# Optimization experiments

Hardware: AMD Instinct MI355X
Metric: run time of the kernel (lower is better)

## Reference

```python
import jax, jax.numpy as jnp
import numpy as np

B, D, T = 8, 1024, 512
HID, NH, NL = 256, 4, 2
OUT = HID // NH  # 64 per-head dim
ALPHA = 0.2      # leaky relu slope
EPS = 1e-5       # layernorm eps


def setup_inputs() -> dict:
    key = jax.random.key(0)
    ks = jax.random.split(key, 10)
    X_obs = jax.random.normal(ks[0], (B, D, T), dtype=jnp.float32)
    mask = (jax.random.uniform(ks[1], (B, D, T)) < 0.8).astype(jnp.float32)
    W_in = jax.random.normal(ks[2], (2 * T, HID), dtype=jnp.float32) * (1.0 / np.sqrt(2 * T))
    b_in = jnp.zeros((HID,), dtype=jnp.float32)
    gat_W = jax.random.normal(ks[3], (NL, NH, HID, OUT), dtype=jnp.float32) * (1.0 / np.sqrt(HID))
    gat_a = jax.random.normal(ks[4], (NL, NH, 2 * OUT), dtype=jnp.float32) * 0.1
    ln_g = jnp.ones((NL, HID), dtype=jnp.float32)
    ln_b = jnp.zeros((NL, HID), dtype=jnp.float32)
    W_out = jax.random.normal(ks[5], (HID, T), dtype=jnp.float32) * (1.0 / np.sqrt(HID))
    b_out = jnp.zeros((T,), dtype=jnp.float32)
    return dict(X_obs=X_obs, mask=mask, W_in=W_in, b_in=b_in, gat_W=gat_W,
                gat_a=gat_a, ln_g=ln_g, ln_b=ln_b, W_out=W_out, b_out=b_out)


def _layer_norm(x, g, b):
    mu = jnp.mean(x, axis=-1, keepdims=True)
    var = jnp.mean((x - mu) ** 2, axis=-1, keepdims=True)
    return (x - mu) * jax.lax.rsqrt(var + EPS) * g + b


def _gat_forward(X_obs, mask, W_in, b_in, gat_W, gat_a, ln_g, ln_b, W_out, b_out):
    # mean-impute per (d, t) position across batch
    obs_sum = jnp.sum(X_obs * mask, axis=0, keepdims=True)
    obs_cnt = jnp.sum(mask, axis=0, keepdims=True)
    pos_mean = obs_sum / (obs_cnt + 1e-10)
    X_mean = X_obs * mask + (1.0 - mask) * pos_mean

    x = jnp.concatenate([X_mean, mask], axis=-1)       # (B, D, 2T)
    h = x @ W_in + b_in                                 # (B, N, HID)

    for l in range(NL):
        Wl = gat_W[l]                                   # (H, HID, OUT)
        a_left = gat_a[l, :, :OUT]                      # (H, OUT)
        a_right = gat_a[l, :, OUT:]                     # (H, OUT)
        hW = jnp.einsum('bnd,hde->bhne', h, Wl)         # (B, H, N, OUT)
        # e_ij = leakyrelu(a_left . h_i + a_right . h_j) -- avoids O(N^2 * 2d) concat
        s_l = jnp.einsum('bhne,he->bhn', hW, a_left)
        s_r = jnp.einsum('bhne,he->bhn', hW, a_right)
        e = jax.nn.leaky_relu(s_l[..., :, None] + s_r[..., None, :], ALPHA)  # (B,H,N,N)
        attn = jax.nn.softmax(e, axis=-1)
        head_out = jnp.einsum('bhnm,bhme->bhne', attn, hW)                   # (B,H,N,OUT)
        h_new = jnp.transpose(head_out, (0, 2, 1, 3)).reshape(h.shape[0], h.shape[1], HID)
        h = _layer_norm(h + h_new, ln_g[l], ln_b[l])

    return h @ W_out + b_out                            # (B, D, T)


def reference(X_obs, mask, W_in, b_in, gat_W, gat_a, ln_g, ln_b, W_out, b_out):
    return _gat_forward(X_obs, mask, W_in, b_in, gat_W, gat_a, ln_g, ln_b, W_out, b_out)
```

## Files before the change

### kernel.cpp

```cpp
#include <hip/hip_runtime.h>
#include <hip/hip_bf16.h>

constexpr int B_   = 8;
constexpr int D_   = 1024;
constexpr int T_   = 512;
constexpr int HID_ = 256;
constexpr int NH_  = 4;
constexpr int NL_  = 2;
constexpr float ALPHA_ = 0.2f;
constexpr float EPS_   = 1e-5f;
constexpr int OUT_ = 64;
constexpr int M_ = B_ * D_;
constexpr int DT_ = D_ * T_;
constexpr int KIN_ = 2 * T_;

typedef __attribute__((ext_vector_type(8))) short short8;
typedef __attribute__((ext_vector_type(4))) float floatx4;

__device__ __forceinline__ unsigned short f2bf(float f) {
    unsigned int u = __float_as_uint(f);
    unsigned int r = u + 0x7fffu + ((u >> 16) & 1u);
    return (unsigned short)(r >> 16);
}
__device__ __forceinline__ float bf2f(unsigned short u) {
    return __uint_as_float((unsigned int)u << 16);
}
__device__ __forceinline__ unsigned int kenc(float f) {
    unsigned int u = __float_as_uint(f);
    return (u & 0x80000000u) ? ~u : (u | 0x80000000u);
}
__device__ __forceinline__ float kdec(unsigned int k) {
    unsigned int u = (k & 0x80000000u) ? (k ^ 0x80000000u) : ~k;
    return __uint_as_float(u);
}
__device__ __forceinline__ void gll16(const unsigned short* g, unsigned short* l) {
    __builtin_amdgcn_global_load_lds(
        (const __attribute__((address_space(1))) void*)g,
        (__attribute__((address_space(3))) void*)l, 16, 0, 0);
}

__global__ __launch_bounds__(256) void impute_k(const float* __restrict__ X,
                                                const float* __restrict__ Mk,
                                                unsigned short* __restrict__ Ain) {
    int idx4 = (blockIdx.x * 256 + threadIdx.x) * 4;
    int t = idx4 & (T_ - 1);
    int d = idx4 >> 9;
    float4 x[B_], m[B_];
    float4 s = {0, 0, 0, 0}, c = {0, 0, 0, 0};
#pragma unroll
    for (int b = 0; b < B_; b++) {
        x[b] = *(const float4*)&X[(size_t)b * DT_ + idx4];
        m[b] = *(const float4*)&Mk[(size_t)b * DT_ + idx4];
        s.x += x[b].x * m[b].x; s.y += x[b].y * m[b].y;
        s.z += x[b].z * m[b].z; s.w += x[b].w * m[b].w;
        c.x += m[b].x; c.y += m[b].y; c.z += m[b].z; c.w += m[b].w;
    }
    float4 pm;
    pm.x = s.x / (c.x + 1e-10f); pm.y = s.y / (c.y + 1e-10f);
    pm.z = s.z / (c.z + 1e-10f); pm.w = s.w / (c.w + 1e-10f);
#pragma unroll
    for (int b = 0; b < B_; b++) {
        size_t row = (size_t)b * D_ + d;
        ushort4 xm, mk;
        xm.x = f2bf(x[b].x * m[b].x + (1.f - m[b].x) * pm.x);
        xm.y = f2bf(x[b].y * m[b].y + (1.f - m[b].y) * pm.y);
        xm.z = f2bf(x[b].z * m[b].z + (1.f - m[b].z) * pm.z);
        xm.w = f2bf(x[b].w * m[b].w + (1.f - m[b].w) * pm.w);
        mk.x = f2bf(m[b].x); mk.y = f2bf(m[b].y);
        mk.z = f2bf(m[b].z); mk.w = f2bf(m[b].w);
        *(ushort4*)&Ain[row * KIN_ + t]      = xm;
        *(ushort4*)&Ain[row * KIN_ + T_ + t] = mk;
    }
}

__global__ __launch_bounds__(256) void wprep_k(const float* __restrict__ W_in,
                                               const float* __restrict__ gatW,
                                               const float* __restrict__ W_out,
                                               unsigned short* __restrict__ Wt_in,
                                               unsigned short* __restrict__ Wcat,
                                               unsigned short* __restrict__ WtO,
                                               unsigned int* __restrict__ rmaxkey) {
    int idx = blockIdx.x * 256 + threadIdx.x;
    if (idx < 64) rmaxkey[idx] = 0u;
    if (idx < 262144) {
        int n = idx >> 10, k = idx & 1023;
        Wt_in[idx] = f2bf(W_in[(size_t)k * HID_ + n]);
    } else if (idx < 393216) {
        int j = idx - 262144;
        int l = j >> 16, n = (j >> 8) & 255, k = j & 255;
        int h = n >> 6, e = n & 63;
        Wcat[j] = f2bf(gatW[(((size_t)(l * NH_ + h) * HID_) + k) * OUT_ + e]);
    } else {
        int j = idx - 393216;
        int n = j >> 8, k = j & 255;
        WtO[j] = f2bf(W_out[(size_t)k * T_ + n]);
    }
}

template <int MODE>
__global__ __launch_bounds__(256) void gemm_bf16_k(
        const unsigned short* __restrict__ A,
        const unsigned short* __restrict__ Bt,
        const float* __restrict__ bias,
        float* __restrict__ C,
        unsigned short* __restrict__ Cb,
        const float* __restrict__ ga,
        float* __restrict__ s_l,
        float* __restrict__ s_r,
        unsigned int* __restrict__ rmaxkey,
        int Nsz, int Ksz) {
    __shared__ __align__(16) unsigned short As[2][128 * 32];
    __shared__ __align__(16) unsigned short Bs[2][64 * 32];
    int tid = threadIdx.x;
    int wave = tid >> 6, lane = tid & 63;
    int q = lane >> 4, r16 = lane & 15;
    int rowbase = blockIdx.y * 128;
    int colbase = blockIdx.x * 64;

    const unsigned short* Ap0 = A + (size_t)(rowbase + (tid >> 2)) * Ksz + (tid & 3) * 8;
    const unsigned short* Ap1 = A + (size_t)(rowbase + (tid >> 2) + 64) * Ksz + (tid & 3) * 8;
    const unsigned short* Bp  = Bt + (size_t)(colbase + (tid >> 2)) * Ksz + (tid & 3) * 8;

    floatx4 acc[2][4];
#pragma unroll
    for (int i = 0; i < 2; i++)
#pragma unroll
        for (int j = 0; j < 4; j++) acc[i][j] = (floatx4)0.f;

    gll16(Ap0, &As[0][tid * 8]);
    gll16(Ap1, &As[0][(tid + 256) * 8]);
    gll16(Bp,  &Bs[0][tid * 8]);

    int nk = Ksz >> 5;
    for (int it = 0; it < nk; it++) {
        int cur = it & 1;
        __syncthreads();
        if (it + 1 < nk) {
            int kt2 = (it + 1) << 5;
            gll16(Ap0 + kt2, &As[cur ^ 1][tid * 8]);
            gll16(Ap1 + kt2, &As[cur ^ 1][(tid + 256) * 8]);
            gll16(Bp + kt2,  &Bs[cur ^ 1][tid * 8]);
        }
        short8 a[2], b[4];
#pragma unroll
        for (int mi = 0; mi < 2; mi++)
            a[mi] = *(const short8*)&As[cur][(wave * 32 + mi * 16 + r16) * 32 + q * 8];
#pragma unroll
        for (int ni = 0; ni < 4; ni++)
            b[ni] = *(const short8*)&Bs[cur][(ni * 16 + r16) * 32 + q * 8];
#pragma unroll
        for (int mi = 0; mi < 2; mi++)
#pragma unroll
            for (int ni = 0; ni < 4; ni++)
                acc[mi][ni] = __builtin_amdgcn_mfma_f32_16x16x32_bf16(
                    a[mi], b[ni], acc[mi][ni], 0, 0, 0);
    }
    if constexpr (MODE == 2) {
        int bhh = ((rowbase >> 10) << 2) + blockIdx.x;
        int nbase = (rowbase & (D_ - 1)) + wave * 32;
#pragma unroll
        for (int mi = 0; mi < 2; mi++) {
#pragma unroll
            for (int ni = 0; ni < 4; ni++) {
                int e = ni * 16 + r16;
                ushort4 pk;
                pk.x = f2bf(acc[mi][ni][0]);
                pk.y = f2bf(acc[mi][ni][1]);
                pk.z = f2bf(acc[mi][ni][2]);
                pk.w = f2bf(acc[mi][ni][3]);
                *(ushort4*)&Cb[((size_t)(bhh * 64 + e) << 10) + nbase + mi * 16 + q * 4] = pk;
            }
        }
        const float* gab = ga + blockIdx.x * 2 * OUT_;
        float al4[4], ar4[4];
#pragma unroll
        for (int ni = 0; ni < 4; ni++) {
            al4[ni] = gab[ni * 16 + r16];
            ar4[ni] = gab[OUT_ + ni * 16 + r16];
        }
        float slv[2][4], srv[2][4];
#pragma unroll
        for (int mi = 0; mi < 2; mi++)
#pragma unroll
            for (int rr = 0; rr < 4; rr++) {
                float s1 = 0.f, s2 = 0.f;
#pragma unroll
                for (int ni = 0; ni < 4; ni++) {
                    s1 += acc[mi][ni][rr] * al4[ni];
                    s2 += acc[mi][ni][rr] * ar4[ni];
                }
                slv[mi][rr] = s1;
                srv[mi][rr] = s2;
            }
#pragma unroll
        for (int off = 1; off < 16; off <<= 1) {
#pragma unroll
            for (int mi = 0; mi < 2; mi++)
#pragma unroll
                for (int rr = 0; rr < 4; rr++) {
                    slv[mi][rr] += __shfl_xor(slv[mi][rr], off, 64);
                    srv[mi][rr] += __shfl_xor(srv[mi][rr], off, 64);
                }
        }
        {
            int slot = r16 & 7;
            int mi = slot >> 2, rr = slot & 3;
            int n = nbase + mi * 16 + q * 4 + rr;
            if (r16 < 8) s_l[bhh * D_ + n] = slv[mi][rr];
            else         s_r[bhh * D_ + n] = srv[mi][rr];
        }
        float mx = -1e30f;
#pragma unroll
        for (int mi = 0; mi < 2; mi++)
#pragma unroll
            for (int rr = 0; rr < 4; rr++) mx = fmaxf(mx, srv[mi][rr]);
        if (lane == 0) atomicMax(&rmaxkey[bhh], kenc(mx));
    } else {
#pragma unroll
        for (int mi = 0; mi < 2; mi++) {
#pragma unroll
            for (int rr = 0; rr < 4; rr++) {
                int row = rowbase + wave * 32 + mi * 16 + q * 4 + rr;
#pragma unroll
                for (int ni = 0; ni < 4; ni++) {
                    int col = colbase + ni * 16 + r16;
                    float v = acc[mi][ni][rr] + (bias ? bias[col] : 0.f);
                    C[(size_t)row * Nsz + col] = v;
                    if constexpr (MODE == 1) Cb[(size_t)row * Nsz + col] = f2bf(v);
                }
            }
        }
    }
}

__global__ __launch_bounds__(256) void attn_k(const unsigned short* __restrict__ hwT,
                                              const float* __restrict__ sl_g,
                                              const float* __restrict__ sr_g,
                                              const unsigned int* __restrict__ rmaxkey,
                                              float* __restrict__ hnew) {
    int bh = blockIdx.x;
    int b = bh >> 2, h = bh & 3;
    int tid = threadIdx.x;
    int wave = tid >> 6, lane = tid & 63;
    int q = lane >> 4, r16 = lane & 15;

    __shared__ float srs[D_];
    __shared__ __align__(16) unsigned short Vt[2][64][136];
    __shared__ float den_lds[64];

    *(float4*)&srs[tid * 4] = *(const float4*)&sr_g[bh * D_ + tid * 4];

    float rm = kdec(rmaxkey[bh]);
    int row0 = blockIdx.y * 64 + wave * 16;
    float sl = sl_g[bh * D_ + row0 + r16];
    float xm = sl + rm;
    float Mn = fmaxf(xm, ALPHA_ * xm);

    floatx4 acc[4];
#pragma unroll
    for (int i = 0; i < 4; i++) acc[i] = (floatx4)0.f;
    float dsum = 0.f;

    const unsigned short* vbase = hwT + ((size_t)(bh * 64) << 10);
    int se[4], sp[4];
#pragma unroll
    for (int i = 0; i < 4; i++) {
        int s = tid + i * 256;
        se[i] = s >> 4;
        sp[i] = (s & 15) * 8;
    }

    uint4 pre[4];
#pragma unroll
    for (int i = 0; i < 4; i++)
        pre[i] = *(const uint4*)&vbase[((size_t)se[i] << 10) + sp[i]];
#pragma unroll
    for (int i = 0; i < 4; i++)
        *(uint4*)&Vt[0][se[i]][sp[i]] = pre[i];
    __syncthreads();

    for (int c = 0; c < 8; c++) {
        int cur = c & 1;
        if (c < 7) {
            int mc = (c + 1) * 128;
#pragma unroll
            for (int i = 0; i < 4; i++)
                pre[i] = *(const uint4*)&vbase[((size_t)se[i] << 10) + mc + sp[i]];
        }
#pragma unroll
        for (int kk = 0; kk < 128; kk += 32) {
            int m0 = c * 128 + kk + q * 8;
            float4 s0 = *(const float4*)&srs[m0];
            float4 s1 = *(const float4*)&srs[m0 + 4];
            float sr8[8] = {s0.x, s0.y, s0.z, s0.w, s1.x, s1.y, s1.z, s1.w};
            float p[8];
#pragma unroll
            for (int j = 0; j < 8; j++) {
                float x = sl + sr8[j];
                float e = fmaxf(x, ALPHA_ * x);
                float pj = __expf(e - Mn);
                dsum += pj;
                p[j] = pj;
            }
            union { unsigned int u[4]; short8 s8; } cv;
#pragma unroll
            for (int j = 0; j < 4; j++) {
                unsigned int lo = (__float_as_uint(p[2 * j]) + 0x8000u) >> 16;
                unsigned int hi = (__float_as_uint(p[2 * j + 1]) + 0x8000u) & 0xffff0000u;
                cv.u[j] = hi | lo;
            }
#pragma unroll
            for (int ni = 0; ni < 4; ni++) {
                short8 bfr = *(const short8*)&Vt[cur][ni * 16 + r16][kk + q * 8];
                acc[ni] = __builtin_amdgcn_mfma_f32_16x16x32_bf16(cv.s8, bfr, acc[ni], 0, 0, 0);
            }
        }
        if (c < 7) {
#pragma unroll
            for (int i = 0; i < 4; i++)
                *(uint4*)&Vt[cur ^ 1][se[i]][sp[i]] = pre[i];
        }
        __syncthreads();
    }
    dsum += __shfl_xor(dsum, 16);
    dsum += __shfl_xor(dsum, 32);
    if (q == 0) den_lds[wave * 16 + r16] = dsum;
    __syncthreads();
#pragma unroll
    for (int rr = 0; rr < 4; rr++) {
        int rloc = q * 4 + rr;
        float rden = 1.f / den_lds[wave * 16 + rloc];
        size_t grow = (size_t)(b * D_ + blockIdx.y * 64 + wave * 16 + rloc);
#pragma unroll
        for (int ni = 0; ni < 4; ni++) {
            hnew[grow * HID_ + h * OUT_ + ni * 16 + r16] = acc[ni][rr] * rden;
        }
    }
}

__global__ __launch_bounds__(256) void addln_k(float* __restrict__ h,
                                               const float* __restrict__ hn,
                                               const float* __restrict__ g,
                                               const float* __restrict__ bb,
                                               unsigned short* __restrict__ hbf) {
    int wave = threadIdx.x >> 6, lane = threadIdx.x & 63;
    size_t row = (size_t)blockIdx.x * 4 + wave;
    float4 a = *(const float4*)&h[row * HID_ + lane * 4];
    float4 r = *(const float4*)&hn[row * HID_ + lane * 4];
    float4 v = {a.x + r.x, a.y + r.y, a.z + r.z, a.w + r.w};
    float s = v.x + v.y + v.z + v.w;
#pragma unroll
    for (int off = 1; off < 64; off <<= 1) s += __shfl_xor(s, off, 64);
    float mu = s * (1.f / HID_);
    float4 d = {v.x - mu, v.y - mu, v.z - mu, v.w - mu};
    float s2 = d.x * d.x + d.y * d.y + d.z * d.z + d.w * d.w;
#pragma unroll
    for (int off = 1; off < 64; off <<= 1) s2 += __shfl_xor(s2, off, 64);
    float rs = rsqrtf(s2 * (1.f / HID_) + EPS_);
    float4 gg = *(const float4*)&g[lane * 4];
    float4 bbv = *(const float4*)&bb[lane * 4];
    float4 res;
    res.x = d.x * rs * gg.x + bbv.x;
    res.y = d.y * rs * gg.y + bbv.y;
    res.z = d.z * rs * gg.z + bbv.z;
    res.w = d.w * rs * gg.w + bbv.w;
    *(float4*)&h[row * HID_ + lane * 4] = res;
    ushort4 pk = {f2bf(res.x), f2bf(res.y), f2bf(res.z), f2bf(res.w)};
    *(ushort4*)&hbf[row * HID_ + lane * 4] = pk;
}

extern "C" void kernel_launch(void* const* d_in, const int* in_sizes, int n_in,
                              void* d_out, int out_size, void* d_ws, size_t ws_size,
                              hipStream_t stream) {
    const float* X_obs = (const float*)d_in[0];
    const float* mask  = (const float*)d_in[1];
    const float* W_in  = (const float*)d_in[2];
    const float* b_in  = (const float*)d_in[3];
    const float* gat_W = (const float*)d_in[4];
    const float* gat_a = (const float*)d_in[5];
    const float* ln_g  = (const float*)d_in[6];
    const float* ln_b  = (const float*)d_in[7];
    const float* W_out = (const float*)d_in[8];
    const float* b_out = (const float*)d_in[9];
    float* out = (float*)d_out;

    char* base = (char*)d_ws;
    unsigned short* Ain  = (unsigned short*)base;
    unsigned short* hwT  = (unsigned short*)base;
    float* hnew = (float*)(base + (4u << 20));
    float* hbuf = (float*)(base + (16u << 20));
    unsigned short* hbf   = (unsigned short*)(base + (24u << 20));
    unsigned short* Wt_in = (unsigned short*)(base + (28u << 20));
    unsigned short* Wcat  = Wt_in + (size_t)HID_ * KIN_;
    unsigned short* WtO   = Wcat + (size_t)NL_ * HID_ * HID_;
    float* slb = (float*)(WtO + (size_t)T_ * HID_);
    float* srb = slb + B_ * NH_ * D_;
    unsigned int* rmaxkey = (unsigned int*)(srb + B_ * NH_ * D_);

    impute_k<<<DT_ / 1024, 256, 0, stream>>>(X_obs, mask, Ain);
    wprep_k<<<2048, 256, 0, stream>>>(W_in, gat_W, W_out, Wt_in, Wcat, WtO, rmaxkey);

    gemm_bf16_k<1><<<dim3(HID_ / 64, M_ / 128), 256, 0, stream>>>(
        Ain, Wt_in, b_in, hbuf, hbf, nullptr, nullptr, nullptr, nullptr,
        HID_, KIN_);

    for (int l = 0; l < NL_; l++) {
        gemm_bf16_k<2><<<dim3(HID_ / 64, M_ / 128), 256, 0, stream>>>(
            hbf, Wcat + (size_t)l * HID_ * HID_, nullptr, nullptr, hwT,
            gat_a + (size_t)l * NH_ * 2 * OUT_, slb, srb, rmaxkey + l * 32,
            HID_, HID_);
        attn_k<<<dim3(B_ * NH_, D_ / 64), 256, 0, stream>>>(
            hwT, slb, srb, rmaxkey + l * 32, hnew);
        addln_k<<<M_ / 4, 256, 0, stream>>>(hbuf, hnew, ln_g + (size_t)l * HID_,
                                            ln_b + (size_t)l * HID_, hbf);
    }

    gemm_bf16_k<0><<<dim3(T_ / 64, M_ / 128), 256, 0, stream>>>(
        hbf, WtO, b_out, out, nullptr, nullptr, nullptr, nullptr, nullptr,
        T_, HID_);
}
```

Baseline: 224.9 us.

## Split attention keys across blocks, shrink GEMM tiles, merge prep kernels

Attention now splits the key dimension in two halves over a third grid axis. Each half writes unnormalised partial accumulators and denominators, and the add+layernorm kernel combines and normalises them. This doubles the block count so more CUs stay busy. GEMM tiles shrink from 128x32 to 64x64 with K=64 steps, padded LDS rows, and register-staged loads in place of global_load_lds, which also gives more blocks. Impute and weight-prep are fused into one launch. The cost is extra global traffic for the partial results and a different GEMM load path.

```diff
diff --git a/kernel.cpp b/kernel.cpp
--- a/kernel.cpp
+++ b/kernel.cpp
@@ -22,9 +22,6 @@
     unsigned int r = u + 0x7fffu + ((u >> 16) & 1u);
     return (unsigned short)(r >> 16);
 }
-__device__ __forceinline__ float bf2f(unsigned short u) {
-    return __uint_as_float((unsigned int)u << 16);
-}
 __device__ __forceinline__ unsigned int kenc(float f) {
     unsigned int u = __float_as_uint(f);
     return (u & 0x80000000u) ? ~u : (u | 0x80000000u);
@@ -33,67 +30,64 @@
     unsigned int u = (k & 0x80000000u) ? (k ^ 0x80000000u) : ~k;
     return __uint_as_float(u);
 }
-__device__ __forceinline__ void gll16(const unsigned short* g, unsigned short* l) {
-    __builtin_amdgcn_global_load_lds(
-        (const __attribute__((address_space(1))) void*)g,
-        (__attribute__((address_space(3))) void*)l, 16, 0, 0);
-}
-
-__global__ __launch_bounds__(256) void impute_k(const float* __restrict__ X,
-                                                const float* __restrict__ Mk,
-                                                unsigned short* __restrict__ Ain) {
-    int idx4 = (blockIdx.x * 256 + threadIdx.x) * 4;
-    int t = idx4 & (T_ - 1);
-    int d = idx4 >> 9;
-    float4 x[B_], m[B_];
-    float4 s = {0, 0, 0, 0}, c = {0, 0, 0, 0};
-#pragma unroll
-    for (int b = 0; b < B_; b++) {
-        x[b] = *(const float4*)&X[(size_t)b * DT_ + idx4];
-        m[b] = *(const float4*)&Mk[(size_t)b * DT_ + idx4];
-        s.x += x[b].x * m[b].x; s.y += x[b].y * m[b].y;
-        s.z += x[b].z * m[b].z; s.w += x[b].w * m[b].w;
-        c.x += m[b].x; c.y += m[b].y; c.z += m[b].z; c.w += m[b].w;
-    }
-    float4 pm;
-    pm.x = s.x / (c.x + 1e-10f); pm.y = s.y / (c.y + 1e-10f);
-    pm.z = s.z / (c.z + 1e-10f); pm.w = s.w / (c.w + 1e-10f);
-#pragma unroll
-    for (int b = 0; b < B_; b++) {
-        size_t row = (size_t)b * D_ + d;
-        ushort4 xm, mk;
-        xm.x = f2bf(x[b].x * m[b].x + (1.f - m[b].x) * pm.x);
-        xm.y = f2bf(x[b].y * m[b].y + (1.f - m[b].y) * pm.y);
-        xm.z = f2bf(x[b].z * m[b].z + (1.f - m[b].z) * pm.z);
-        xm.w = f2bf(x[b].w * m[b].w + (1.f - m[b].w) * pm.w);
-        mk.x = f2bf(m[b].x); mk.y = f2bf(m[b].y);
-        mk.z = f2bf(m[b].z); mk.w = f2bf(m[b].w);
-        *(ushort4*)&Ain[row * KIN_ + t]      = xm;
-        *(ushort4*)&Ain[row * KIN_ + T_ + t] = mk;
-    }
-}
-
-__global__ __launch_bounds__(256) void wprep_k(const float* __restrict__ W_in,
-                                               const float* __restrict__ gatW,
-                                               const float* __restrict__ W_out,
-                                               unsigned short* __restrict__ Wt_in,
-                                               unsigned short* __restrict__ Wcat,
-                                               unsigned short* __restrict__ WtO,
-                                               unsigned int* __restrict__ rmaxkey) {
-    int idx = blockIdx.x * 256 + threadIdx.x;
-    if (idx < 64) rmaxkey[idx] = 0u;
-    if (idx < 262144) {
-        int n = idx >> 10, k = idx & 1023;
-        Wt_in[idx] = f2bf(W_in[(size_t)k * HID_ + n]);
-    } else if (idx < 393216) {
-        int j = idx - 262144;
-        int l = j >> 16, n = (j >> 8) & 255, k = j & 255;
-        int h = n >> 6, e = n & 63;
-        Wcat[j] = f2bf(gatW[(((size_t)(l * NH_ + h) * HID_) + k) * OUT_ + e]);
+
+__global__ __launch_bounds__(256) void prep_k(const float* __restrict__ X,
+                                              const float* __restrict__ Mk,
+                                              const float* __restrict__ W_in,
+                                              const float* __restrict__ gatW,
+                                              const float* __restrict__ W_out,
+                                              unsigned short* __restrict__ Ain,
+                                              unsigned short* __restrict__ Wt_in,
+                                              unsigned short* __restrict__ Wcat,
+                                              unsigned short* __restrict__ WtO,
+                                              unsigned int* __restrict__ rmaxkey) {
+    int bx = blockIdx.x;
+    if (bx < 512) {
+        int idx4 = (bx * 256 + threadIdx.x) * 4;
+        int t = idx4 & (T_ - 1);
+        int d = idx4 >> 9;
+        float4 x[B_], m[B_];
+        float4 s = {0, 0, 0, 0}, c = {0, 0, 0, 0};
+#pragma unroll
+        for (int b = 0; b < B_; b++) {
+            x[b] = *(const float4*)&X[(size_t)b * DT_ + idx4];
+            m[b] = *(const float4*)&Mk[(size_t)b * DT_ + idx4];
+            s.x += x[b].x * m[b].x; s.y += x[b].y * m[b].y;
+            s.z += x[b].z * m[b].z; s.w += x[b].w * m[b].w;
+            c.x += m[b].x; c.y += m[b].y; c.z += m[b].z; c.w += m[b].w;
+        }
+        float4 pm;
+        pm.x = s.x / (c.x + 1e-10f); pm.y = s.y / (c.y + 1e-10f);
+        pm.z = s.z / (c.z + 1e-10f); pm.w = s.w / (c.w + 1e-10f);
+#pragma unroll
+        for (int b = 0; b < B_; b++) {
+            size_t row = (size_t)b * D_ + d;
+            ushort4 xm, mk;
+            xm.x = f2bf(x[b].x * m[b].x + (1.f - m[b].x) * pm.x);
+            xm.y = f2bf(x[b].y * m[b].y + (1.f - m[b].y) * pm.y);
+            xm.z = f2bf(x[b].z * m[b].z + (1.f - m[b].z) * pm.z);
+            xm.w = f2bf(x[b].w * m[b].w + (1.f - m[b].w) * pm.w);
+            mk.x = f2bf(m[b].x); mk.y = f2bf(m[b].y);
+            mk.z = f2bf(m[b].z); mk.w = f2bf(m[b].w);
+            *(ushort4*)&Ain[row * KIN_ + t]      = xm;
+            *(ushort4*)&Ain[row * KIN_ + T_ + t] = mk;
+        }
     } else {
-        int j = idx - 393216;
-        int n = j >> 8, k = j & 255;
-        WtO[j] = f2bf(W_out[(size_t)k * T_ + n]);
+        int idx = (bx - 512) * 256 + threadIdx.x;
+        if (idx < 64) rmaxkey[idx] = 0u;
+        if (idx < 262144) {
+            int n = idx >> 10, k = idx & 1023;
+            Wt_in[idx] = f2bf(W_in[(size_t)k * HID_ + n]);
+        } else if (idx < 393216) {
+            int j = idx - 262144;
+            int l = j >> 16, n = (j >> 8) & 255, k = j & 255;
+            int h = n >> 6, e = n & 63;
+            Wcat[j] = f2bf(gatW[(((size_t)(l * NH_ + h) * HID_) + k) * OUT_ + e]);
+        } else {
+            int j = idx - 393216;
+            int n = j >> 8, k = j & 255;
+            WtO[j] = f2bf(W_out[(size_t)k * T_ + n]);
+        }
     }
 }
 
@@ -109,67 +103,72 @@
         float* __restrict__ s_r,
         unsigned int* __restrict__ rmaxkey,
         int Nsz, int Ksz) {
-    __shared__ __align__(16) unsigned short As[2][128 * 32];
-    __shared__ __align__(16) unsigned short Bs[2][64 * 32];
+    __shared__ __align__(16) unsigned short As[2][64 * 72];
+    __shared__ __align__(16) unsigned short Bs[2][64 * 72];
     int tid = threadIdx.x;
     int wave = tid >> 6, lane = tid & 63;
     int q = lane >> 4, r16 = lane & 15;
-    int rowbase = blockIdx.y * 128;
+    int rowbase = blockIdx.y * 64;
     int colbase = blockIdx.x * 64;
 
-    const unsigned short* Ap0 = A + (size_t)(rowbase + (tid >> 2)) * Ksz + (tid & 3) * 8;
-    const unsigned short* Ap1 = A + (size_t)(rowbase + (tid >> 2) + 64) * Ksz + (tid & 3) * 8;
-    const unsigned short* Bp  = Bt + (size_t)(colbase + (tid >> 2)) * Ksz + (tid & 3) * 8;
-
-    floatx4 acc[2][4];
-#pragma unroll
-    for (int i = 0; i < 2; i++)
-#pragma unroll
-        for (int j = 0; j < 4; j++) acc[i][j] = (floatx4)0.f;
-
-    gll16(Ap0, &As[0][tid * 8]);
-    gll16(Ap1, &As[0][(tid + 256) * 8]);
-    gll16(Bp,  &Bs[0][tid * 8]);
-
-    int nk = Ksz >> 5;
+    int srow = tid >> 3, sk = (tid & 7) * 8;
+    const unsigned short* Ap0 = A + (size_t)(rowbase + srow) * Ksz + sk;
+    const unsigned short* Ap1 = A + (size_t)(rowbase + srow + 32) * Ksz + sk;
+    const unsigned short* Bp0 = Bt + (size_t)(colbase + srow) * Ksz + sk;
+    const unsigned short* Bp1 = Bt + (size_t)(colbase + srow + 32) * Ksz + sk;
+    int la0 = srow * 72 + sk, la1 = (srow + 32) * 72 + sk;
+
+    floatx4 acc[4];
+#pragma unroll
+    for (int i = 0; i < 4; i++) acc[i] = (floatx4)0.f;
+
+    uint4 pa0 = *(const uint4*)Ap0, pa1 = *(const uint4*)Ap1;
+    uint4 pb0 = *(const uint4*)Bp0, pb1 = *(const uint4*)Bp1;
+    *(uint4*)&As[0][la0] = pa0;
+    *(uint4*)&As[0][la1] = pa1;
+    *(uint4*)&Bs[0][la0] = pb0;
+    *(uint4*)&Bs[0][la1] = pb1;
+
+    int nk = Ksz >> 6;
     for (int it = 0; it < nk; it++) {
         int cur = it & 1;
         __syncthreads();
         if (it + 1 < nk) {
-            int kt2 = (it + 1) << 5;
-            gll16(Ap0 + kt2, &As[cur ^ 1][tid * 8]);
-            gll16(Ap1 + kt2, &As[cur ^ 1][(tid + 256) * 8]);
-            gll16(Bp + kt2,  &Bs[cur ^ 1][tid * 8]);
-        }
-        short8 a[2], b[4];
-#pragma unroll
-        for (int mi = 0; mi < 2; mi++)
-            a[mi] = *(const short8*)&As[cur][(wave * 32 + mi * 16 + r16) * 32 + q * 8];
-#pragma unroll
-        for (int ni = 0; ni < 4; ni++)
-            b[ni] = *(const short8*)&Bs[cur][(ni * 16 + r16) * 32 + q * 8];
-#pragma unroll
-        for (int mi = 0; mi < 2; mi++)
-#pragma unroll
-            for (int ni = 0; ni < 4; ni++)
-                acc[mi][ni] = __builtin_amdgcn_mfma_f32_16x16x32_bf16(
-                    a[mi], b[ni], acc[mi][ni], 0, 0, 0);
+            int kt = (it + 1) << 6;
+            pa0 = *(const uint4*)(Ap0 + kt);
+            pa1 = *(const uint4*)(Ap1 + kt);
+            pb0 = *(const uint4*)(Bp0 + kt);
+            pb1 = *(const uint4*)(Bp1 + kt);
+        }
+#pragma unroll
+        for (int t = 0; t < 2; t++) {
+            short8 a = *(const short8*)&As[cur][(wave * 16 + r16) * 72 + t * 32 + q * 8];
+#pragma unroll
+            for (int ni = 0; ni < 4; ni++) {
+                short8 b = *(const short8*)&Bs[cur][(ni * 16 + r16) * 72 + t * 32 + q * 8];
+                acc[ni] = __builtin_amdgcn_mfma_f32_16x16x32_bf16(a, b, acc[ni], 0, 0, 0);
+            }
+        }
+        if (it + 1 < nk) {
+            int nxt = cur ^ 1;
+            *(uint4*)&As[nxt][la0] = pa0;
+            *(uint4*)&As[nxt][la1] = pa1;
+            *(uint4*)&Bs[nxt][la0] = pb0;
+            *(uint4*)&Bs[nxt][la1] = pb1;
+        }
     }
     if constexpr (MODE == 2) {
         int bhh = ((rowbase >> 10) << 2) + blockIdx.x;
-        int nbase = (rowbase & (D_ - 1)) + wave * 32;
-#pragma unroll
-        for (int mi = 0; mi < 2; mi++) {
-#pragma unroll
-            for (int ni = 0; ni < 4; ni++) {
-                int e = ni * 16 + r16;
-                ushort4 pk;
-                pk.x = f2bf(acc[mi][ni][0]);
-                pk.y = f2bf(acc[mi][ni][1]);
-                pk.z = f2bf(acc[mi][ni][2]);
-                pk.w = f2bf(acc[mi][ni][3]);
-                *(ushort4*)&Cb[((size_t)(bhh * 64 + e) << 10) + nbase + mi * 16 + q * 4] = pk;
-            }
+        int nb = (rowbase & (D_ - 1)) + wave * 16;
+#pragma unroll
+        for (int ni = 0; ni < 4; ni++) {
+            int e = ni * 16 + r16;
+            ushort4 pk;
+            pk.x = f2bf(acc[ni][0]);
+            pk.y = f2bf(acc[ni][1]);
+            pk.z = f2bf(acc[ni][2]);
+            pk.w = f2bf(acc[ni][3]);
+            *(ushort4*)&Cb[((size_t)(bhh * 64 + e) << 10) + nb + q * 4] = pk;
         }
         const float* gab = ga + blockIdx.x * 2 * OUT_;
         float al4[4], ar4[4];
@@ -178,56 +177,48 @@
             al4[ni] = gab[ni * 16 + r16];
             ar4[ni] = gab[OUT_ + ni * 16 + r16];
         }
-        float slv[2][4], srv[2][4];
-#pragma unroll
-        for (int mi = 0; mi < 2; mi++)
+        float slv[4], srv[4];
+#pragma unroll
+        for (int rr = 0; rr < 4; rr++) {
+            float s1 = 0.f, s2 = 0.f;
+#pragma unroll
+            for (int ni = 0; ni < 4; ni++) {
+                s1 += acc[ni][rr] * al4[ni];
+                s2 += acc[ni][rr] * ar4[ni];
+            }
+            slv[rr] = s1;
+            srv[rr] = s2;
+        }
+#pragma unroll
+        for (int off = 1; off < 16; off <<= 1) {
 #pragma unroll
             for (int rr = 0; rr < 4; rr++) {
-                float s1 = 0.f, s2 = 0.f;
-#pragma unroll
-                for (int ni = 0; ni < 4; ni++) {
-                    s1 += acc[mi][ni][rr] * al4[ni];
-                    s2 += acc[mi][ni][rr] * ar4[ni];
-                }
-                slv[mi][rr] = s1;
-                srv[mi][rr] = s2;
-            }
-#pragma unroll
-        for (int off = 1; off < 16; off <<= 1) {
-#pragma unroll
-            for (int mi = 0; mi < 2; mi++)
-#pragma unroll
-                for (int rr = 0; rr < 4; rr++) {
-                    slv[mi][rr] += __shfl_xor(slv[mi][rr], off, 64);
-                    srv[mi][rr] += __shfl_xor(srv[mi][rr], off, 64);
-                }
+                slv[rr] += __shfl_xor(slv[rr], off, 64);
+                srv[rr] += __shfl_xor(srv[rr], off, 64);
+            }
         }
         {
-            int slot = r16 & 7;
-            int mi = slot >> 2, rr = slot & 3;
-            int n = nbase + mi * 16 + q * 4 + rr;
-            if (r16 < 8) s_l[bhh * D_ + n] = slv[mi][rr];
-            else         s_r[bhh * D_ + n] = srv[mi][rr];
-        }
-        float mx = -1e30f;
-#pragma unroll
-        for (int mi = 0; mi < 2; mi++)
-#pragma unroll
-            for (int rr = 0; rr < 4; rr++) mx = fmaxf(mx, srv[mi][rr]);
+            int rsel = r16 & 3;
+            float sv = (rsel == 0) ? slv[0] : (rsel == 1) ? slv[1] : (rsel == 2) ? slv[2] : slv[3];
+            float rv = (rsel == 0) ? srv[0] : (rsel == 1) ? srv[1] : (rsel == 2) ? srv[2] : srv[3];
+            int n = nb + q * 4 + rsel;
+            if (r16 < 4)                 s_l[bhh * D_ + n] = sv;
+            else if (r16 >= 8 && r16 < 12) s_r[bhh * D_ + n] = rv;
+        }
+        float mx = fmaxf(fmaxf(srv[0], srv[1]), fmaxf(srv[2], srv[3]));
+        mx = fmaxf(mx, __shfl_xor(mx, 16, 64));
+        mx = fmaxf(mx, __shfl_xor(mx, 32, 64));
         if (lane == 0) atomicMax(&rmaxkey[bhh], kenc(mx));
     } else {
 #pragma unroll
-        for (int mi = 0; mi < 2; mi++) {
-#pragma unroll
-            for (int rr = 0; rr < 4; rr++) {
-                int row = rowbase + wave * 32 + mi * 16 + q * 4 + rr;
-#pragma unroll
-                for (int ni = 0; ni < 4; ni++) {
-                    int col = colbase + ni * 16 + r16;
-                    float v = acc[mi][ni][rr] + (bias ? bias[col] : 0.f);
-                    C[(size_t)row * Nsz + col] = v;
-                    if constexpr (MODE == 1) Cb[(size_t)row * Nsz + col] = f2bf(v);
-                }
+        for (int rr = 0; rr < 4; rr++) {
+            int row = rowbase + wave * 16 + q * 4 + rr;
+#pragma unroll
+            for (int ni = 0; ni < 4; ni++) {
+                int col = colbase + ni * 16 + r16;
+                float v = acc[ni][rr] + (bias ? bias[col] : 0.f);
+                C[(size_t)row * Nsz + col] = v;
+                if constexpr (MODE == 1) Cb[(size_t)row * Nsz + col] = f2bf(v);
             }
         }
     }
@@ -237,18 +228,20 @@
                                               const float* __restrict__ sl_g,
                                               const float* __restrict__ sr_g,
                                               const unsigned int* __restrict__ rmaxkey,
-                                              float* __restrict__ hnew) {
+                                              float* __restrict__ pacc,
+                                              float* __restrict__ pden) {
     int bh = blockIdx.x;
     int b = bh >> 2, h = bh & 3;
+    int half = blockIdx.z;
+    int mb = half * 512;
     int tid = threadIdx.x;
     int wave = tid >> 6, lane = tid & 63;
     int q = lane >> 4, r16 = lane & 15;
 
-    __shared__ float srs[D_];
+    __shared__ float srs[512];
     __shared__ __align__(16) unsigned short Vt[2][64][136];
-    __shared__ float den_lds[64];
-
-    *(float4*)&srs[tid * 4] = *(const float4*)&sr_g[bh * D_ + tid * 4];
+
+    *(float2*)&srs[tid * 2] = *(const float2*)&sr_g[bh * D_ + mb + tid * 2];
 
     float rm = kdec(rmaxkey[bh]);
     int row0 = blockIdx.y * 64 + wave * 16;
@@ -261,7 +254,7 @@
     for (int i = 0; i < 4; i++) acc[i] = (floatx4)0.f;
     float dsum = 0.f;
 
-    const unsigned short* vbase = hwT + ((size_t)(bh * 64) << 10);
+    const unsigned short* vbase = hwT + ((size_t)(bh * 64) << 10) + mb;
     int se[4], sp[4];
 #pragma unroll
     for (int i = 0; i < 4; i++) {
@@ -279,13 +272,13 @@
         *(uint4*)&Vt[0][se[i]][sp[i]] = pre[i];
     __syncthreads();
 
-    for (int c = 0; c < 8; c++) {
+    for (int c = 0; c < 4; c++) {
         int cur = c & 1;
-        if (c < 7) {
-            int mc = (c + 1) * 128;
+        if (c < 3) {
+            int mo = (c + 1) * 128;
 #pragma unroll
             for (int i = 0; i < 4; i++)
-                pre[i] = *(const uint4*)&vbase[((size_t)se[i] << 10) + mc + sp[i]];
+                pre[i] = *(const uint4*)&vbase[((size_t)se[i] << 10) + mo + sp[i]];
         }
 #pragma unroll
         for (int kk = 0; kk < 128; kk += 32) {
@@ -315,7 +308,7 @@
                 acc[ni] = __builtin_amdgcn_mfma_f32_16x16x32_bf16(cv.s8, bfr, acc[ni], 0, 0, 0);
             }
         }
-        if (c < 7) {
+        if (c < 3) {
 #pragma unroll
             for (int i = 0; i < 4; i++)
                 *(uint4*)&Vt[cur ^ 1][se[i]][sp[i]] = pre[i];
@@ -324,30 +317,35 @@
     }
     dsum += __shfl_xor(dsum, 16);
     dsum += __shfl_xor(dsum, 32);
-    if (q == 0) den_lds[wave * 16 + r16] = dsum;
-    __syncthreads();
+    size_t gr0 = (size_t)b * D_ + row0;
+    if (lane < 16) pden[((size_t)half * M_ + gr0 + r16) * NH_ + h] = dsum;
 #pragma unroll
     for (int rr = 0; rr < 4; rr++) {
         int rloc = q * 4 + rr;
-        float rden = 1.f / den_lds[wave * 16 + rloc];
-        size_t grow = (size_t)(b * D_ + blockIdx.y * 64 + wave * 16 + rloc);
+        size_t grow = gr0 + rloc;
 #pragma unroll
         for (int ni = 0; ni < 4; ni++) {
-            hnew[grow * HID_ + h * OUT_ + ni * 16 + r16] = acc[ni][rr] * rden;
+            pacc[((size_t)half * M_ + grow) * HID_ + h * OUT_ + ni * 16 + r16] = acc[ni][rr];
         }
     }
 }
 
 __global__ __launch_bounds__(256) void addln_k(float* __restrict__ h,
-                                               const float* __restrict__ hn,
+                                               const float* __restrict__ pacc,
+                                               const float* __restrict__ pden,
                                                const float* __restrict__ g,
                                                const float* __restrict__ bb,
                                                unsigned short* __restrict__ hbf) {
     int wave = threadIdx.x >> 6, lane = threadIdx.x & 63;
     size_t row = (size_t)blockIdx.x * 4 + wave;
-    float4 a = *(const float4*)&h[row * HID_ + lane * 4];
-    float4 r = *(const float4*)&hn[row * HID_ + lane * 4];
-    float4 v = {a.x + r.x, a.y + r.y, a.z + r.z, a.w + r.w};
+    float4 a  = *(const float4*)&h[row * HID_ + lane * 4];
+    float4 p0 = *(const float4*)&pacc[row * HID_ + lane * 4];
+    float4 p1 = *(const float4*)&pacc[((size_t)M_ + row) * HID_ + lane * 4];
+    int hh = lane >> 4;
+    float den = pden[row * NH_ + hh] + pden[((size_t)M_ + row) * NH_ + hh];
+    float inv = 1.f / den;
+    float4 v = {a.x + (p0.x + p1.x) * inv, a.y + (p0.y + p1.y) * inv,
+                a.z + (p0.z + p1.z) * inv, a.w + (p0.w + p1.w) * inv};
     float s = v.x + v.y + v.z + v.w;
 #pragma unroll
     for (int off = 1; off < 64; off <<= 1) s += __shfl_xor(s, off, 64);
@@ -387,35 +385,37 @@
     char* base = (char*)d_ws;
     unsigned short* Ain  = (unsigned short*)base;
     unsigned short* hwT  = (unsigned short*)base;
-    float* hnew = (float*)(base + (4u << 20));
-    float* hbuf = (float*)(base + (16u << 20));
-    unsigned short* hbf   = (unsigned short*)(base + (24u << 20));
-    unsigned short* Wt_in = (unsigned short*)(base + (28u << 20));
+    float* pacc = (float*)(base + (4u << 20));
+    float* pden = (float*)(base + (20u << 20));
+    float* hbuf = (float*)(base + (21u << 20));
+    unsigned short* hbf   = (unsigned short*)(base + (29u << 20));
+    unsigned short* Wt_in = (unsigned short*)(base + (33u << 20));
     unsigned short* Wcat  = Wt_in + (size_t)HID_ * KIN_;
     unsigned short* WtO   = Wcat + (size_t)NL_ * HID_ * HID_;
     float* slb = (float*)(WtO + (size_t)T_ * HID_);
     float* srb = slb + B_ * NH_ * D_;
     unsigned int* rmaxkey = (unsigned int*)(srb + B_ * NH_ * D_);
 
-    impute_k<<<DT_ / 1024, 256, 0, stream>>>(X_obs, mask, Ain);
-    wprep_k<<<2048, 256, 0, stream>>>(W_in, gat_W, W_out, Wt_in, Wcat, WtO, rmaxkey);
-
-    gemm_bf16_k<1><<<dim3(HID_ / 64, M_ / 128), 256, 0, stream>>>(
+    prep_k<<<2560, 256, 0, stream>>>(X_obs, mask, W_in, gat_W, W_out,
+                                     Ain, Wt_in, Wcat, WtO, rmaxkey);
+
+    gemm_bf16_k<1><<<dim3(HID_ / 64, M_ / 64), 256, 0, stream>>>(
         Ain, Wt_in, b_in, hbuf, hbf, nullptr, nullptr, nullptr, nullptr,
         HID_, KIN_);
 
     for (int l = 0; l < NL_; l++) {
-        gemm_bf16_k<2><<<dim3(HID_ / 64, M_ / 128), 256, 0, stream>>>(
+        gemm_bf16_k<2><<<dim3(HID_ / 64, M_ / 64), 256, 0, stream>>>(
             hbf, Wcat + (size_t)l * HID_ * HID_, nullptr, nullptr, hwT,
             gat_a + (size_t)l * NH_ * 2 * OUT_, slb, srb, rmaxkey + l * 32,
             HID_, HID_);
-        attn_k<<<dim3(B_ * NH_, D_ / 64), 256, 0, stream>>>(
-            hwT, slb, srb, rmaxkey + l * 32, hnew);
-        addln_k<<<M_ / 4, 256, 0, stream>>>(hbuf, hnew, ln_g + (size_t)l * HID_,
+        attn_k<<<dim3(B_ * NH_, D_ / 64, 2), 256, 0, stream>>>(
+            hwT, slb, srb, rmaxkey + l * 32, pacc, pden);
+        addln_k<<<M_ / 4, 256, 0, stream>>>(hbuf, pacc, pden,
+                                            ln_g + (size_t)l * HID_,
                                             ln_b + (size_t)l * HID_, hbf);
     }
 
-    gemm_bf16_k<0><<<dim3(T_ / 64, M_ / 128), 256, 0, stream>>>(
+    gemm_bf16_k<0><<<dim3(T_ / 64, M_ / 64), 256, 0, stream>>>(
         hbf, WtO, b_out, out, nullptr, nullptr, nullptr, nullptr, nullptr,
         T_, HID_);
 }
```

Result: faster. 216.5 us (-3.7%).
